# Kernel optimization log

Hardware: AMD Instinct MI355X
Metric: run time of the kernel (lower is better)

The kernel has to match this reference:

```python
import jax, jax.numpy as jnp
import numpy as np

NUM_USERS = 100000
NUM_ITEMS = 100000
EMB_DIM = 64
NUM_NODES = NUM_USERS + NUM_ITEMS
NUM_EDGES = 4000000
BATCH = 4096
NUM_LAYERS = 2


def setup_inputs() -> dict:
    key = jax.random.key(0)
    ks = jax.random.split(key, 8)
    user = jax.random.randint(ks[0], (BATCH,), 0, NUM_USERS, dtype=jnp.int64) if jax.config.jax_enable_x64 else jax.random.randint(ks[0], (BATCH,), 0, NUM_USERS, dtype=jnp.int32)
    pos = jax.random.randint(ks[1], (BATCH,), 0, NUM_ITEMS, dtype=jnp.int32)
    neg = jax.random.randint(ks[2], (BATCH,), 0, NUM_ITEMS, dtype=jnp.int32)
    edge_row = jax.random.randint(ks[3], (NUM_EDGES,), 0, NUM_NODES, dtype=jnp.int32)
    edge_col = jax.random.randint(ks[4], (NUM_EDGES,), 0, NUM_NODES, dtype=jnp.int32)
    # normalized adjacency values (degree-normalized in real LightGCN)
    edge_val = jax.random.uniform(ks[5], (NUM_EDGES,), dtype=jnp.float32) * 0.01
    user_emb = jax.random.normal(ks[6], (NUM_USERS, EMB_DIM), dtype=jnp.float32) * 0.01
    item_emb = jax.random.normal(ks[7], (NUM_ITEMS, EMB_DIM), dtype=jnp.float32) * 0.01
    return {"user": user, "pos": pos, "neg": neg,
            "edge_row": edge_row, "edge_col": edge_col, "edge_val": edge_val,
            "user_emb": user_emb, "item_emb": item_emb}


def _spmm(edge_row, edge_col, edge_val, x):
    # out[r] = sum_e val[e] * x[col[e]]  -- sparse adjacency times dense emb
    msgs = edge_val[:, None] * x[edge_col]  # [E, D]
    return jax.ops.segment_sum(msgs, edge_row, num_segments=NUM_NODES)


def reference(user, pos, neg, edge_row, edge_col, edge_val, user_emb, item_emb):
    all_emb = jnp.concatenate([user_emb, item_emb], axis=0)  # [N, D]
    acc = all_emb
    h = all_emb
    for _ in range(NUM_LAYERS):
        h = _spmm(edge_row, edge_col, edge_val, h)
        acc = acc + h
    lightgcn_out = acc / (NUM_LAYERS + 1)  # mean over stacked layer embeddings
    u = lightgcn_out[:NUM_USERS]
    i = lightgcn_out[NUM_USERS:]
    user_latent = u[user]          # [B, D]
    positive_latent = i[pos]       # [B, D]
    negative_latent = i[neg]       # [B, D]
    positive_score = jnp.sum(user_latent * positive_latent, axis=1)
    negative_score = jnp.sum(user_latent * negative_latent, axis=1)
    return positive_score, negative_score
```

## Files before the change

### kernel.cpp

```cpp
#include <hip/hip_runtime.h>
#include <cstdint>
#include <cstddef>

#define NUM_USERS 100000
#define NUM_ITEMS 100000
#define NUM_NODES 200000
#define NUM_EDGES 4000000
#define BATCH     4096
#define EMB       64

#define RPB   512
#define NB    391
#define CAP   11264
#define CHUNK 16384
#define PTHREADS 1024
#define EPB   16



__device__ __forceinline__ unsigned short f2bf(float f) {
    unsigned u = __float_as_uint(f);
    u = (u + 0x7FFFu + ((u >> 16) & 1u)) >> 16;
    return (unsigned short)u;
}
__device__ __forceinline__ float bf2f(unsigned short b) {
    return __uint_as_float(((unsigned)b) << 16);
}
__device__ __forceinline__ float bflo(unsigned u) { return __uint_as_float(u << 16); }
__device__ __forceinline__ float bfhi(unsigned u) { return __uint_as_float(u & 0xFFFF0000u); }
__device__ __forceinline__ unsigned pack2(float a, float b) {
    return (unsigned)f2bf(a) | ((unsigned)f2bf(b) << 16);
}


__global__ void k_part1(const int* __restrict__ erow, const int* __restrict__ ecol,
                        const float* __restrict__ eval_, int* __restrict__ bcur,
                        int2* __restrict__ tmp) {
    __shared__ int hist[NB];
    __shared__ int base[NB];
    int t = threadIdx.x;
    int start = blockIdx.x * CHUNK;
    for (int i = t; i < NB; i += PTHREADS) hist[i] = 0;
    __syncthreads();
    int rows[EPB], ranks[EPB];
#pragma unroll
    for (int k = 0; k < EPB; ++k) {
        int e = start + t + k * PTHREADS;
        if (e < NUM_EDGES) {
            int r = erow[e];
            rows[k]  = r;
            ranks[k] = atomicAdd(&hist[r >> 9], 1);
        } else {
            rows[k] = -1;
        }
    }
    __syncthreads();
    for (int i = t; i < NB; i += PTHREADS) {
        int c = hist[i];
        base[i] = c ? atomicAdd(&bcur[i], c) : 0;
    }
    __syncthreads();
#pragma unroll
    for (int k = 0; k < EPB; ++k) {
        int e = start + t + k * PTHREADS;
        if (rows[k] >= 0) {
            int r   = rows[k];
            int bkt = r >> 9;
            int pos = bkt * CAP + base[bkt] + ranks[k];
            if (pos < (bkt + 1) * CAP)
                tmp[pos] = make_int2(((r & 511) << 18) | ecol[e], __float_as_int(eval_[e]));
        }
    }
}


__global__ void k_part2(const int* __restrict__ bcur, const int2* __restrict__ tmp,
                        int2* __restrict__ epack, int2* __restrict__ rowext,
                        const float* __restrict__ uemb, const float* __restrict__ iemb,
                        unsigned short* __restrict__ xb) {
    __shared__ int cnt[RPB];
    __shared__ int sc[RPB];
    __shared__ int loc[RPB];
    int b = blockIdx.x, t = threadIdx.x;

    const int TOT8 = (NUM_NODES * EMB) / 8;
    const int PER  = (TOT8 + NB - 1) / NB;
    int u0 = b * PER, u1 = min(u0 + PER, TOT8);
    const size_t UELEMS = (size_t)NUM_USERS * EMB;
    for (int u = u0 + t; u < u1; u += 512) {
        size_t off = (size_t)u * 8;
        const float* src = (off < UELEMS) ? (uemb + off) : (iemb + (off - UELEMS));
        float4 f0 = ((const float4*)src)[0];
        float4 f1 = ((const float4*)src)[1];
        ushort4 o0 = make_ushort4(f2bf(f0.x), f2bf(f0.y), f2bf(f0.z), f2bf(f0.w));
        ushort4 o1 = make_ushort4(f2bf(f1.x), f2bf(f1.y), f2bf(f1.z), f2bf(f1.w));
        ((ushort4*)(xb + off))[0] = o0;
        ((ushort4*)(xb + off))[1] = o1;
    }

    int base_row = b << 9;
    int nrows = min(RPB, NUM_NODES - base_row);
    int s0 = b * CAP;
    int n = min(bcur[b], CAP);
    cnt[t] = 0;
    __syncthreads();
    for (int i = t; i < n; i += 512)
        atomicAdd(&cnt[((unsigned)tmp[s0 + i].x) >> 18], 1);
    __syncthreads();
    int v = cnt[t];
    sc[t] = v;
    __syncthreads();
    for (int off = 1; off < RPB; off <<= 1) {
        int add = (t >= off) ? sc[t - off] : 0;
        __syncthreads();
        sc[t] += add;
        __syncthreads();
    }
    int cur = s0 + sc[t] - v;
    if (t < nrows) rowext[base_row + t] = make_int2(cur, v);
    loc[t] = cur;
    __syncthreads();
    for (int i = t; i < n; i += 512) {
        int2 rec = tmp[s0 + i];
        int pos = atomicAdd(&loc[((unsigned)rec.x) >> 18], 1);
        epack[pos] = make_int2(rec.x & 0x3FFFF, rec.y);
    }
}


__global__ void k_spmm1(const int2* __restrict__ rowext, const int2* __restrict__ epack,
                        const unsigned short* __restrict__ xb,
                        unsigned short* __restrict__ h1) {
    int wid  = (blockIdx.x * blockDim.x + threadIdx.x) >> 6;
    int lane = threadIdx.x & 63;
    if (wid >= NUM_NODES) return;
    int g = lane >> 3;
    int q = (lane & 7) * 8;
    int2 se = rowext[wid];
    int s = se.x, t = se.x + se.y;
    float a0 = 0.f, a1 = 0.f, a2 = 0.f, a3 = 0.f;
    float a4 = 0.f, a5 = 0.f, a6 = 0.f, a7 = 0.f;
    for (int e = s; e < t; e += 8) {
        int idx = e + g;
        int2 p = epack[idx < t ? idx : s];
        float v = (idx < t) ? __int_as_float(p.y) : 0.f;
        uint4 X = *(const uint4*)(xb + (size_t)p.x * EMB + q);
        a0 = fmaf(v, bflo(X.x), a0); a1 = fmaf(v, bfhi(X.x), a1);
        a2 = fmaf(v, bflo(X.y), a2); a3 = fmaf(v, bfhi(X.y), a3);
        a4 = fmaf(v, bflo(X.z), a4); a5 = fmaf(v, bfhi(X.z), a5);
        a6 = fmaf(v, bflo(X.w), a6); a7 = fmaf(v, bfhi(X.w), a7);
    }
#pragma unroll
    for (int off = 8; off < 64; off <<= 1) {
        a0 += __shfl_xor(a0, off, 64); a1 += __shfl_xor(a1, off, 64);
        a2 += __shfl_xor(a2, off, 64); a3 += __shfl_xor(a3, off, 64);
        a4 += __shfl_xor(a4, off, 64); a5 += __shfl_xor(a5, off, 64);
        a6 += __shfl_xor(a6, off, 64); a7 += __shfl_xor(a7, off, 64);
    }
    if (lane < 8) {
        uint4 o = make_uint4(pack2(a0, a1), pack2(a2, a3), pack2(a4, a5), pack2(a6, a7));
        *(uint4*)(h1 + (size_t)wid * EMB + q) = o;
    }
}


__device__ __forceinline__ const float* node_ptr(int c, const float* __restrict__ uemb,
                                                 const float* __restrict__ iemb) {
    return (c < NUM_USERS) ? (uemb + (size_t)c * EMB)
                           : (iemb + (size_t)(c - NUM_USERS) * EMB);
}

__global__ void k_final(const int* __restrict__ user, const int* __restrict__ pos,
                        const int* __restrict__ neg,
                        const int2* __restrict__ rowext, const int2* __restrict__ epack,
                        const float* __restrict__ uemb, const float* __restrict__ iemb,
                        const unsigned short* __restrict__ h1, float* __restrict__ out) {
    __shared__ float lds[3 * EMB];
    int b    = blockIdx.x;
    int w    = threadIdx.x >> 6;
    int lane = threadIdx.x & 63;
    int g = lane >> 3;
    int q = (lane & 7) * 8;

    int node;
    if (w == 0)      node = user[b];
    else if (w == 1) node = NUM_USERS + pos[b];
    else             node = NUM_USERS + neg[b];

    int2 se = rowext[node];
    int s = se.x, t = se.x + se.y;
    float a0 = 0.f, a1 = 0.f, a2 = 0.f, a3 = 0.f;
    float a4 = 0.f, a5 = 0.f, a6 = 0.f, a7 = 0.f;
    for (int e = s; e < t; e += 8) {
        int idx = e + g;
        int2 p = epack[idx < t ? idx : s];
        float v = (idx < t) ? __int_as_float(p.y) : 0.f;
        uint4 Y = *(const uint4*)(h1 + (size_t)p.x * EMB + q);
        a0 = fmaf(v, bflo(Y.x), a0); a1 = fmaf(v, bfhi(Y.x), a1);
        a2 = fmaf(v, bflo(Y.y), a2); a3 = fmaf(v, bfhi(Y.y), a3);
        a4 = fmaf(v, bflo(Y.z), a4); a5 = fmaf(v, bfhi(Y.z), a5);
        a6 = fmaf(v, bflo(Y.w), a6); a7 = fmaf(v, bfhi(Y.w), a7);
    }
#pragma unroll
    for (int off = 8; off < 64; off <<= 1) {
        a0 += __shfl_xor(a0, off, 64); a1 += __shfl_xor(a1, off, 64);
        a2 += __shfl_xor(a2, off, 64); a3 += __shfl_xor(a3, off, 64);
        a4 += __shfl_xor(a4, off, 64); a5 += __shfl_xor(a5, off, 64);
        a6 += __shfl_xor(a6, off, 64); a7 += __shfl_xor(a7, off, 64);
    }

    if (lane < 8) {
        const float* xbp = node_ptr(node, uemb, iemb) + q;
        float4 xd0 = ((const float4*)xbp)[0];
        float4 xd1 = ((const float4*)xbp)[1];
        uint4  hn  = *(const uint4*)(h1 + (size_t)node * EMB + q);
        a0 = (a0 + xd0.x + bflo(hn.x)) / 3.0f;
        a1 = (a1 + xd0.y + bfhi(hn.x)) / 3.0f;
        a2 = (a2 + xd0.z + bflo(hn.y)) / 3.0f;
        a3 = (a3 + xd0.w + bfhi(hn.y)) / 3.0f;
        a4 = (a4 + xd1.x + bflo(hn.z)) / 3.0f;
        a5 = (a5 + xd1.y + bfhi(hn.z)) / 3.0f;
        a6 = (a6 + xd1.z + bflo(hn.w)) / 3.0f;
        a7 = (a7 + xd1.w + bfhi(hn.w)) / 3.0f;
        float* dst = lds + w * EMB + q;
        dst[0] = a0; dst[1] = a1; dst[2] = a2; dst[3] = a3;
        dst[4] = a4; dst[5] = a5; dst[6] = a6; dst[7] = a7;
    }
    __syncthreads();

    if (w < 2) {
        float prod = lds[lane] * lds[(w + 1) * EMB + lane];
        for (int off = 32; off; off >>= 1) prod += __shfl_xor(prod, off, 64);
        if (lane == 0) out[w * BATCH + b] = prod;
    }
}


extern "C" void kernel_launch(void* const* d_in, const int* in_sizes, int n_in,
                              void* d_out, int out_size, void* d_ws, size_t ws_size,
                              hipStream_t stream) {
    const int*   user  = (const int*)d_in[0];
    const int*   pos   = (const int*)d_in[1];
    const int*   neg   = (const int*)d_in[2];
    const int*   erow  = (const int*)d_in[3];
    const int*   ecol  = (const int*)d_in[4];
    const float* eval_ = (const float*)d_in[5];
    const float* uemb  = (const float*)d_in[6];
    const float* iemb  = (const float*)d_in[7];
    float* out = (float*)d_out;

    char* ws = (char*)d_ws;
    unsigned short* xb = (unsigned short*)(ws);
    unsigned short* h1 = (unsigned short*)(ws + 25600000);
    int2* tmp     = (int2*)(ws + 25600000);
    int2* rowext  = (int2*)(ws + 60833792);
    int*  bcur    = (int*)(ws + 62433792);
    int2* epack   = (int2*)(ws + 62437888);

    hipMemsetAsync(bcur, 0, NB * sizeof(int), stream);

    k_part1<<<(NUM_EDGES + CHUNK - 1) / CHUNK, PTHREADS, 0, stream>>>(erow, ecol, eval_,
                                                                      bcur, tmp);

    k_part2<<<NB, RPB, 0, stream>>>(bcur, tmp, epack, rowext, uemb, iemb, xb);

    k_spmm1<<<(NUM_NODES * 64 + 255) / 256, 256, 0, stream>>>(rowext, epack, xb, h1);

    k_final<<<BATCH, 192, 0, stream>>>(user, pos, neg, rowext, epack,
                                       uemb, iemb, h1, out);
}
```

Measured before the change: 346.8 us.

## Sub-sort edges by column slice within rows and split bf16 conversion into own kernel

Edges within each row are now bucketed by the high bits of the column index (8 slices), so the per-row edge list is roughly ordered by source node. This is meant to improve locality of the embedding gathers in the SpMM kernels. The fp32-to-bf16 conversion of embeddings moves out of k_part2 into a separate k_cvt kernel that also zeroes the bucket counters, replacing the memset. The trade-offs are an extra kernel launch, a larger shared histogram, and the conversion no longer being overlapped with the partition work.

```diff
diff --git a/kernel.cpp b/kernel.cpp
--- a/kernel.cpp
+++ b/kernel.cpp
@@ -15,6 +15,8 @@
 #define CHUNK 16384
 #define PTHREADS 1024
 #define EPB   16
+#define NSLICE 8
+#define NBINS (RPB * NSLICE)
 
 
 
@@ -30,6 +32,24 @@
 __device__ __forceinline__ float bfhi(unsigned u) { return __uint_as_float(u & 0xFFFF0000u); }
 __device__ __forceinline__ unsigned pack2(float a, float b) {
     return (unsigned)f2bf(a) | ((unsigned)f2bf(b) << 16);
+}
+
+
+__global__ void k_cvt(const float* __restrict__ uemb, const float* __restrict__ iemb,
+                      unsigned short* __restrict__ xb, int* __restrict__ bcur) {
+    int i = blockIdx.x * blockDim.x + threadIdx.x;
+    if (i < NB) bcur[i] = 0;
+    const int TOT8 = (NUM_NODES * EMB) / 8;
+    if (i >= TOT8) return;
+    size_t off = (size_t)i * 8;
+    const size_t UELEMS = (size_t)NUM_USERS * EMB;
+    const float* src = (off < UELEMS) ? (uemb + off) : (iemb + (off - UELEMS));
+    float4 f0 = ((const float4*)src)[0];
+    float4 f1 = ((const float4*)src)[1];
+    ushort4 o0 = make_ushort4(f2bf(f0.x), f2bf(f0.y), f2bf(f0.z), f2bf(f0.w));
+    ushort4 o1 = make_ushort4(f2bf(f1.x), f2bf(f1.y), f2bf(f1.z), f2bf(f1.w));
+    ((ushort4*)(xb + off))[0] = o0;
+    ((ushort4*)(xb + off))[1] = o1;
 }
 
 
@@ -75,40 +95,31 @@
 
 
 __global__ void k_part2(const int* __restrict__ bcur, const int2* __restrict__ tmp,
-                        int2* __restrict__ epack, int2* __restrict__ rowext,
-                        const float* __restrict__ uemb, const float* __restrict__ iemb,
-                        unsigned short* __restrict__ xb) {
-    __shared__ int cnt[RPB];
+                        int2* __restrict__ epack, int2* __restrict__ rowext) {
+    __shared__ int cnt[NBINS];
     __shared__ int sc[RPB];
-    __shared__ int loc[RPB];
     int b = blockIdx.x, t = threadIdx.x;
-
-    const int TOT8 = (NUM_NODES * EMB) / 8;
-    const int PER  = (TOT8 + NB - 1) / NB;
-    int u0 = b * PER, u1 = min(u0 + PER, TOT8);
-    const size_t UELEMS = (size_t)NUM_USERS * EMB;
-    for (int u = u0 + t; u < u1; u += 512) {
-        size_t off = (size_t)u * 8;
-        const float* src = (off < UELEMS) ? (uemb + off) : (iemb + (off - UELEMS));
-        float4 f0 = ((const float4*)src)[0];
-        float4 f1 = ((const float4*)src)[1];
-        ushort4 o0 = make_ushort4(f2bf(f0.x), f2bf(f0.y), f2bf(f0.z), f2bf(f0.w));
-        ushort4 o1 = make_ushort4(f2bf(f1.x), f2bf(f1.y), f2bf(f1.z), f2bf(f1.w));
-        ((ushort4*)(xb + off))[0] = o0;
-        ((ushort4*)(xb + off))[1] = o1;
-    }
-
     int base_row = b << 9;
     int nrows = min(RPB, NUM_NODES - base_row);
     int s0 = b * CAP;
     int n = min(bcur[b], CAP);
-    cnt[t] = 0;
-    __syncthreads();
-    for (int i = t; i < n; i += 512)
-        atomicAdd(&cnt[((unsigned)tmp[s0 + i].x) >> 18], 1);
-    __syncthreads();
-    int v = cnt[t];
-    sc[t] = v;
+
+#pragma unroll
+    for (int j = 0; j < NSLICE; ++j) cnt[t * NSLICE + j] = 0;
+    __syncthreads();
+    for (int i = t; i < n; i += RPB) {
+        int x = tmp[s0 + i].x;
+        atomicAdd(&cnt[((x >> 18) << 3) | ((x & 0x3FFFF) >> 15)], 1);
+    }
+    __syncthreads();
+    int c[NSLICE], ex[NSLICE], tot = 0;
+#pragma unroll
+    for (int j = 0; j < NSLICE; ++j) {
+        c[j]  = cnt[t * NSLICE + j];
+        ex[j] = tot;
+        tot  += c[j];
+    }
+    sc[t] = tot;
     __syncthreads();
     for (int off = 1; off < RPB; off <<= 1) {
         int add = (t >= off) ? sc[t - off] : 0;
@@ -116,14 +127,16 @@
         sc[t] += add;
         __syncthreads();
     }
-    int cur = s0 + sc[t] - v;
-    if (t < nrows) rowext[base_row + t] = make_int2(cur, v);
-    loc[t] = cur;
-    __syncthreads();
-    for (int i = t; i < n; i += 512) {
+    int rbase = sc[t] - tot;
+#pragma unroll
+    for (int j = 0; j < NSLICE; ++j) cnt[t * NSLICE + j] = s0 + rbase + ex[j];
+    if (t < nrows) rowext[base_row + t] = make_int2(s0 + rbase, tot);
+    __syncthreads();
+    for (int i = t; i < n; i += RPB) {
         int2 rec = tmp[s0 + i];
-        int pos = atomicAdd(&loc[((unsigned)rec.x) >> 18], 1);
-        epack[pos] = make_int2(rec.x & 0x3FFFF, rec.y);
+        int x = rec.x;
+        int pos = atomicAdd(&cnt[((x >> 18) << 3) | ((x & 0x3FFFF) >> 15)], 1);
+        epack[pos] = make_int2(x & 0x3FFFF, rec.y);
     }
 }
 
@@ -257,12 +270,12 @@
     int*  bcur    = (int*)(ws + 62433792);
     int2* epack   = (int2*)(ws + 62437888);
 
-    hipMemsetAsync(bcur, 0, NB * sizeof(int), stream);
+    k_cvt<<<((NUM_NODES * EMB) / 8 + 255) / 256, 256, 0, stream>>>(uemb, iemb, xb, bcur);
 
     k_part1<<<(NUM_EDGES + CHUNK - 1) / CHUNK, PTHREADS, 0, stream>>>(erow, ecol, eval_,
                                                                       bcur, tmp);
 
-    k_part2<<<NB, RPB, 0, stream>>>(bcur, tmp, epack, rowext, uemb, iemb, xb);
+    k_part2<<<NB, RPB, 0, stream>>>(bcur, tmp, epack, rowext);
 
     k_spmm1<<<(NUM_NODES * 64 + 255) / 256, 256, 0, stream>>>(rowext, epack, xb, h1);
 
```

New measurement: 352.7 us. No clear change (+1.7%).

## Halve bucket size to 256 rows and move bf16 conversion into partition pass

Applied to the files above, without the earlier changes.

The bucket sort now uses 782 buckets of 256 rows instead of 391 buckets of 512, doubling the number of second-pass blocks. Each second-pass block therefore handles less work and the pass has more parallelism. The fp32-to-bf16 embedding conversion moves from the second pass into the first, with packed 16-byte stores. k_part2 still launches 512 threads but only 256 take part in the scan, so half of each block sits idle during that phase.

```diff
diff --git a/kernel.cpp b/kernel.cpp
--- a/kernel.cpp
+++ b/kernel.cpp
@@ -9,12 +9,12 @@
 #define BATCH     4096
 #define EMB       64
 
-#define RPB   512
-#define NB    391
-#define CAP   11264
+#define NB    782
+#define CAP   5632
 #define CHUNK 16384
 #define PTHREADS 1024
 #define EPB   16
+#define NBLK1 245
 
 
 
@@ -23,9 +23,6 @@
     u = (u + 0x7FFFu + ((u >> 16) & 1u)) >> 16;
     return (unsigned short)u;
 }
-__device__ __forceinline__ float bf2f(unsigned short b) {
-    return __uint_as_float(((unsigned)b) << 16);
-}
 __device__ __forceinline__ float bflo(unsigned u) { return __uint_as_float(u << 16); }
 __device__ __forceinline__ float bfhi(unsigned u) { return __uint_as_float(u & 0xFFFF0000u); }
 __device__ __forceinline__ unsigned pack2(float a, float b) {
@@ -35,7 +32,9 @@
 
 __global__ void k_part1(const int* __restrict__ erow, const int* __restrict__ ecol,
                         const float* __restrict__ eval_, int* __restrict__ bcur,
-                        int2* __restrict__ tmp) {
+                        int2* __restrict__ tmp,
+                        const float* __restrict__ uemb, const float* __restrict__ iemb,
+                        unsigned short* __restrict__ xb) {
     __shared__ int hist[NB];
     __shared__ int base[NB];
     int t = threadIdx.x;
@@ -49,7 +48,7 @@
         if (e < NUM_EDGES) {
             int r = erow[e];
             rows[k]  = r;
-            ranks[k] = atomicAdd(&hist[r >> 9], 1);
+            ranks[k] = atomicAdd(&hist[r >> 8], 1);
         } else {
             rows[k] = -1;
         }
@@ -65,65 +64,64 @@
         int e = start + t + k * PTHREADS;
         if (rows[k] >= 0) {
             int r   = rows[k];
-            int bkt = r >> 9;
+            int bkt = r >> 8;
             int pos = bkt * CAP + base[bkt] + ranks[k];
             if (pos < (bkt + 1) * CAP)
-                tmp[pos] = make_int2(((r & 511) << 18) | ecol[e], __float_as_int(eval_[e]));
+                tmp[pos] = make_int2(((r & 255) << 24) | ecol[e], __float_as_int(eval_[e]));
         }
     }
-}
-
-
-__global__ void k_part2(const int* __restrict__ bcur, const int2* __restrict__ tmp,
-                        int2* __restrict__ epack, int2* __restrict__ rowext,
-                        const float* __restrict__ uemb, const float* __restrict__ iemb,
-                        unsigned short* __restrict__ xb) {
-    __shared__ int cnt[RPB];
-    __shared__ int sc[RPB];
-    __shared__ int loc[RPB];
-    int b = blockIdx.x, t = threadIdx.x;
 
     const int TOT8 = (NUM_NODES * EMB) / 8;
-    const int PER  = (TOT8 + NB - 1) / NB;
-    int u0 = b * PER, u1 = min(u0 + PER, TOT8);
+    const int PER  = (TOT8 + NBLK1 - 1) / NBLK1;
+    int u0 = blockIdx.x * PER, u1 = min(u0 + PER, TOT8);
     const size_t UELEMS = (size_t)NUM_USERS * EMB;
-    for (int u = u0 + t; u < u1; u += 512) {
+    for (int u = u0 + t; u < u1; u += PTHREADS) {
         size_t off = (size_t)u * 8;
         const float* src = (off < UELEMS) ? (uemb + off) : (iemb + (off - UELEMS));
         float4 f0 = ((const float4*)src)[0];
         float4 f1 = ((const float4*)src)[1];
-        ushort4 o0 = make_ushort4(f2bf(f0.x), f2bf(f0.y), f2bf(f0.z), f2bf(f0.w));
-        ushort4 o1 = make_ushort4(f2bf(f1.x), f2bf(f1.y), f2bf(f1.z), f2bf(f1.w));
-        ((ushort4*)(xb + off))[0] = o0;
-        ((ushort4*)(xb + off))[1] = o1;
-    }
-
-    int base_row = b << 9;
-    int nrows = min(RPB, NUM_NODES - base_row);
+        uint4 o = make_uint4(pack2(f0.x, f0.y), pack2(f0.z, f0.w),
+                             pack2(f1.x, f1.y), pack2(f1.z, f1.w));
+        *(uint4*)(xb + off) = o;
+    }
+}
+
+
+__global__ void k_part2(const int* __restrict__ bcur, const int2* __restrict__ tmp,
+                        int2* __restrict__ epack, int2* __restrict__ rowext) {
+    __shared__ int cnt[256];
+    __shared__ int sc[256];
+    __shared__ int loc[256];
+    int b = blockIdx.x, t = threadIdx.x;
+    int base_row = b << 8;
+    int nrows = min(256, NUM_NODES - base_row);
     int s0 = b * CAP;
     int n = min(bcur[b], CAP);
-    cnt[t] = 0;
+    if (t < 256) cnt[t] = 0;
     __syncthreads();
     for (int i = t; i < n; i += 512)
-        atomicAdd(&cnt[((unsigned)tmp[s0 + i].x) >> 18], 1);
-    __syncthreads();
-    int v = cnt[t];
-    sc[t] = v;
-    __syncthreads();
-    for (int off = 1; off < RPB; off <<= 1) {
-        int add = (t >= off) ? sc[t - off] : 0;
+        atomicAdd(&cnt[((unsigned)tmp[s0 + i].x) >> 24], 1);
+    __syncthreads();
+    int v = 0;
+    if (t < 256) { v = cnt[t]; sc[t] = v; }
+    __syncthreads();
+    for (int off = 1; off < 256; off <<= 1) {
+        int add = 0;
+        if (t < 256 && t >= off) add = sc[t - off];
         __syncthreads();
-        sc[t] += add;
+        if (t < 256 && t >= off) sc[t] += add;
         __syncthreads();
     }
-    int cur = s0 + sc[t] - v;
-    if (t < nrows) rowext[base_row + t] = make_int2(cur, v);
-    loc[t] = cur;
+    if (t < 256) {
+        int cur = s0 + sc[t] - v;
+        if (t < nrows) rowext[base_row + t] = make_int2(cur, v);
+        loc[t] = cur;
+    }
     __syncthreads();
     for (int i = t; i < n; i += 512) {
         int2 rec = tmp[s0 + i];
-        int pos = atomicAdd(&loc[((unsigned)rec.x) >> 18], 1);
-        epack[pos] = make_int2(rec.x & 0x3FFFF, rec.y);
+        int pos = atomicAdd(&loc[((unsigned)rec.x) >> 24], 1);
+        epack[pos] = make_int2(rec.x & 0xFFFFFF, rec.y);
     }
 }
 
@@ -259,10 +257,10 @@
 
     hipMemsetAsync(bcur, 0, NB * sizeof(int), stream);
 
-    k_part1<<<(NUM_EDGES + CHUNK - 1) / CHUNK, PTHREADS, 0, stream>>>(erow, ecol, eval_,
-                                                                      bcur, tmp);
-
-    k_part2<<<NB, RPB, 0, stream>>>(bcur, tmp, epack, rowext, uemb, iemb, xb);
+    k_part1<<<NBLK1, PTHREADS, 0, stream>>>(erow, ecol, eval_, bcur, tmp,
+                                            uemb, iemb, xb);
+
+    k_part2<<<NB, 512, 0, stream>>>(bcur, tmp, epack, rowext);
 
     k_spmm1<<<(NUM_NODES * 64 + 255) / 256, 256, 0, stream>>>(rowext, epack, xb, h1);
 
```

New measurement: 358.0 us. 3.2% more time.
